# Kernel tuning notes

Hardware: AMD Instinct MI355X
Metric: run time of the kernel (lower is better)

The kernel has to match this reference:

```python
import jax, jax.numpy as jnp
import numpy as np

SPLIT = 8            # square window (split_size=[8,8], idx 0/1 identical)
DIM = 192
HEADS = 8
NH = HEADS // 2      # heads per branch
CH = DIM // 2        # channels per branch
HD = CH // NH        # head dim = 24
POS_DIM = (CH // 4) // 4  # DynamicPosBias hidden = 6
SCALE = HD ** -0.5
N = SPLIT * SPLIT    # window token count = 64


def _rel_index():
    c = np.arange(SPLIT)
    coords = np.stack(np.meshgrid(c, c, indexing='ij')).reshape(2, -1)
    rel = (coords[:, :, None] - coords[:, None, :]).transpose(1, 2, 0)
    rel[:, :, 0] += SPLIT - 1
    rel[:, :, 1] += SPLIT - 1
    rel[:, :, 0] *= 2 * SPLIT - 1
    return rel.sum(-1).reshape(-1)  # (N*N,) in [0, (2*SPLIT-1)^2)


def _rpe_biases():
    h = np.arange(1 - SPLIT, SPLIT)
    b = np.stack(np.meshgrid(h, h, indexing='ij')).reshape(2, -1).T
    return b.astype(np.float32)  # ((2*SPLIT-1)^2, 2) = (225, 2)


def _layernorm(x, g, b):
    mu = x.mean(-1, keepdims=True)
    var = ((x - mu) ** 2).mean(-1, keepdims=True)
    return (x - mu) / jnp.sqrt(var + 1e-5) * g + b


def setup_inputs() -> dict:
    key = jax.random.key(0)
    ks = jax.random.split(key, 12)
    s = 0.02
    inp = {
        'x': jax.random.normal(ks[0], (2, 65536, DIM), jnp.float32),
        'qkv_w': jax.random.normal(ks[1], (3 * DIM, DIM), jnp.float32) * s,
        'proj_w': jax.random.normal(ks[2], (DIM, DIM), jnp.float32) * s,
        'proj_b': jnp.zeros((DIM,), jnp.float32),
        # DynamicPosBias params, stacked over the 2 branches
        'pos_proj_w': jax.random.normal(ks[3], (2, POS_DIM, 2), jnp.float32) * s,
        'pos_proj_b': jnp.zeros((2, POS_DIM), jnp.float32),
        'ln1_g': jnp.ones((2, POS_DIM), jnp.float32),
        'ln1_b': jnp.zeros((2, POS_DIM), jnp.float32),
        'fc1_w': jax.random.normal(ks[4], (2, POS_DIM, POS_DIM), jnp.float32) * s,
        'fc1_b': jnp.zeros((2, POS_DIM), jnp.float32),
        'ln2_g': jnp.ones((2, POS_DIM), jnp.float32),
        'ln2_b': jnp.zeros((2, POS_DIM), jnp.float32),
        'fc2_w': jax.random.normal(ks[5], (2, POS_DIM, POS_DIM), jnp.float32) * s,
        'fc2_b': jnp.zeros((2, POS_DIM), jnp.float32),
        'ln3_g': jnp.ones((2, POS_DIM), jnp.float32),
        'ln3_b': jnp.zeros((2, POS_DIM), jnp.float32),
        'fc3_w': jax.random.normal(ks[6], (2, NH, POS_DIM), jnp.float32) * s,
        'fc3_b': jnp.zeros((2, NH), jnp.float32),
        'H': 256,
        'W': 256,
    }
    return inp


def reference(x, qkv_w, proj_w, proj_b, pos_proj_w, pos_proj_b,
              ln1_g, ln1_b, fc1_w, fc1_b, ln2_g, ln2_b, fc2_w, fc2_b,
              ln3_g, ln3_b, fc3_w, fc3_b, H, W):
    B, L, C = x.shape
    assert L == H * W and H % SPLIT == 0 and W % SPLIT == 0
    qkv = (x @ qkv_w.T).reshape(B, L, 3, C).transpose(2, 0, 1, 3)  # (3,B,L,C)
    rel_idx = jnp.asarray(_rel_index())
    rpe = jnp.asarray(_rpe_biases())
    outs = []
    for i in range(2):  # two channel-split branches
        qkv_i = qkv[..., i * CH:(i + 1) * CH]  # (3,B,L,CH)
        # window partition: (B,L,CH) -> (B*nW, NH, N, HD)
        def im2win(t):
            t = t.reshape(B, H // SPLIT, SPLIT, W // SPLIT, SPLIT, CH)
            t = t.transpose(0, 1, 3, 2, 4, 5).reshape(-1, N, NH, HD)
            return t.transpose(0, 2, 1, 3)
        q, k, v = im2win(qkv_i[0]), im2win(qkv_i[1]), im2win(qkv_i[2])
        attn = jnp.einsum('whnd,whmd->whnm', q * SCALE, k)  # (B*nW, NH, N, N)
        # dynamic relative position bias MLP (residual=False): pos3(pos2(pos1(proj(b))))
        pos = rpe @ pos_proj_w[i].T + pos_proj_b[i]
        pos = jax.nn.relu(_layernorm(pos, ln1_g[i], ln1_b[i])) @ fc1_w[i].T + fc1_b[i]
        pos = jax.nn.relu(_layernorm(pos, ln2_g[i], ln2_b[i])) @ fc2_w[i].T + fc2_b[i]
        pos = jax.nn.relu(_layernorm(pos, ln3_g[i], ln3_b[i])) @ fc3_w[i].T + fc3_b[i]  # (225, NH)
        bias = pos[rel_idx].reshape(N, N, NH).transpose(2, 0, 1)  # (NH, N, N)
        attn = jax.nn.softmax(attn + bias[None], axis=-1)
        o = jnp.einsum('whnm,whmd->whnd', attn, v)  # (B*nW, NH, N, HD)
        # windows2img back to (B, L, CH)
        o = o.transpose(0, 2, 1, 3).reshape(B, H // SPLIT, W // SPLIT, SPLIT, SPLIT, CH)
        o = o.transpose(0, 1, 3, 2, 4, 5).reshape(B, L, CH)
        outs.append(o)
    out = jnp.concatenate(outs, axis=-1)
    return out @ proj_w.T + proj_b
```

## Files before the change

### kernel.cpp

```cpp
#include <hip/hip_runtime.h>

typedef unsigned short u16;
typedef unsigned int u32;
typedef short short8v __attribute__((ext_vector_type(8)));
typedef float float4v __attribute__((ext_vector_type(4)));
typedef unsigned short ushort4v __attribute__((ext_vector_type(4)));

#define XLD   216
#define C1LD  392
#define VSLD  72
#define PLD   72
#define VS_OFF (64*C1LD)
#define LDS_U16 (VS_OFF + 8*24*VSLD)
#define LDS_BYTES (LDS_U16*2)

#define SC2 (0.20412414523193154f * 1.4426950408889634f)

__device__ __forceinline__ u16 f2bf(float f){
  unsigned u = __builtin_bit_cast(unsigned, f);
  return (u16)((u + 0x7FFFu + ((u >> 16) & 1u)) >> 16);
}
__device__ __forceinline__ void st4(u16* p, float4v v){
  ushort4v pk = { f2bf(v[0]), f2bf(v[1]), f2bf(v[2]), f2bf(v[3]) };
  *(ushort4v*)p = pk;
}

__global__ void prep_convert(const float* __restrict__ qkv_w, const float* __restrict__ proj_w,
                             u16* __restrict__ Wq, u16* __restrict__ Wp){
  int idx = blockIdx.x*blockDim.x + threadIdx.x;
  const int total = 110592 + 36864;
  for (; idx < total; idx += gridDim.x*blockDim.x){
    if (idx < 110592) Wq[idx] = f2bf(qkv_w[idx]);
    else              Wp[idx-110592] = f2bf(proj_w[idx-110592]);
  }
}

__device__ __forceinline__ void lnrelu6(float* v, const float* g, const float* b){
  float mu = (v[0]+v[1]+v[2]+v[3]+v[4]+v[5]) * (1.0f/6.0f);
  float var = 0.f;
  #pragma unroll
  for (int j=0;j<6;++j){ float d = v[j]-mu; var += d*d; }
  var *= (1.0f/6.0f);
  float inv = rsqrtf(var + 1e-5f);
  #pragma unroll
  for (int j=0;j<6;++j) v[j] = fmaxf((v[j]-mu)*inv*g[j] + b[j], 0.f);
}

__global__ void prep_bias(const float* __restrict__ ppw, const float* __restrict__ ppb,
                          const float* __restrict__ ln1g, const float* __restrict__ ln1b,
                          const float* __restrict__ fc1w, const float* __restrict__ fc1b,
                          const float* __restrict__ ln2g, const float* __restrict__ ln2b,
                          const float* __restrict__ fc2w, const float* __restrict__ fc2b,
                          const float* __restrict__ ln3g, const float* __restrict__ ln3b,
                          const float* __restrict__ fc3w, const float* __restrict__ fc3b,
                          float* __restrict__ biasT){
  __shared__ float pos3[2][225][4];
  const int t = threadIdx.x;
  if (t < 225){
    const float dy = (float)(t/15) - 7.0f;
    const float dx = (float)(t%15) - 7.0f;
    for (int i=0;i<2;++i){
      float v[6], y[6];
      #pragma unroll
      for (int j=0;j<6;++j)
        v[j] = dy*ppw[(i*6+j)*2+0] + dx*ppw[(i*6+j)*2+1] + ppb[i*6+j];
      lnrelu6(v, ln1g+i*6, ln1b+i*6);
      #pragma unroll
      for (int j=0;j<6;++j){
        float a = fc1b[i*6+j];
        #pragma unroll
        for (int k=0;k<6;++k) a += v[k]*fc1w[(i*6+j)*6+k];
        y[j] = a;
      }
      lnrelu6(y, ln2g+i*6, ln2b+i*6);
      #pragma unroll
      for (int j=0;j<6;++j){
        float a = fc2b[i*6+j];
        #pragma unroll
        for (int k=0;k<6;++k) a += y[k]*fc2w[(i*6+j)*6+k];
        v[j] = a;
      }
      lnrelu6(v, ln3g+i*6, ln3b+i*6);
      #pragma unroll
      for (int h=0;h<4;++h){
        float a = fc3b[i*4+h];
        #pragma unroll
        for (int k=0;k<6;++k) a += v[k]*fc3w[(i*4+h)*6+k];
        pos3[i][t][h] = a * 1.4426950408889634f;
      }
    }
  }
  __syncthreads();
  for (int idx = t; idx < 32768; idx += 256){
    int i  = idx >> 14;
    int hh = (idx >> 12) & 3;
    int n  = (idx >> 6) & 63;
    int m  = idx & 63;
    int tt = (((n>>3)-(m>>3)+7)*15) + ((n&7)-(m&7)+7);
    biasT[idx] = pos3[i][tt][hh];
  }
}

__device__ __forceinline__ void attn_head(u16* lds, u16* P,
                                          const short8v* qf, const short8v* kf,
                                          const float4v* bv, int hp, int q16, int g,
                                          float4v (&oo)[2][4]){
  const short8v z8 = {0,0,0,0,0,0,0,0};
  float4v s[4][4];
  #pragma unroll
  for (int kt=0;kt<4;++kt)
    #pragma unroll
    for (int mt=0;mt<4;++mt)
      s[kt][mt] = (float4v){0.f,0.f,0.f,0.f};
  __builtin_amdgcn_s_setprio(1);
  #pragma unroll
  for (int kt=0;kt<4;++kt)
    #pragma unroll
    for (int mt=0;mt<4;++mt)
      s[kt][mt] = __builtin_amdgcn_mfma_f32_16x16x32_bf16(kf[kt], qf[mt], s[kt][mt], 0,0,0);
  __builtin_amdgcn_s_setprio(0);
  #pragma unroll
  for (int kt=0;kt<4;++kt)
    #pragma unroll
    for (int mt=0;mt<4;++mt)
      s[kt][mt] = s[kt][mt]*SC2 + bv[kt*4+mt];
  float inv[4];
  #pragma unroll
  for (int mt=0;mt<4;++mt){
    float mx = s[0][mt][0];
    #pragma unroll
    for (int kt=0;kt<4;++kt)
      #pragma unroll
      for (int r=0;r<4;++r) mx = fmaxf(mx, s[kt][mt][r]);
    mx = fmaxf(mx, __shfl_xor(mx, 16));
    mx = fmaxf(mx, __shfl_xor(mx, 32));
    float sum = 0.f;
    #pragma unroll
    for (int kt=0;kt<4;++kt){
      float4v ev;
      #pragma unroll
      for (int r=0;r<4;++r){ float t2 = exp2f(s[kt][mt][r]-mx); ev[r] = t2; sum += t2; }
      st4(&P[(mt*16+q16)*PLD + kt*16 + g*4], ev);
    }
    sum += __shfl_xor(sum, 16);
    sum += __shfl_xor(sum, 32);
    inv[mt] = 1.0f / sum;
  }
  asm volatile("" ::: "memory");
  short8v vf[2][2];
  #pragma unroll
  for (int dt=0;dt<2;++dt){
    const int d  = dt*16 + q16;
    const int dc = (d < 24) ? d : 0;
    #pragma unroll
    for (int kc=0;kc<2;++kc){
      short8v vv = *(const short8v*)&lds[VS_OFF + (hp*24 + dc)*VSLD + kc*32 + g*8];
      vf[dt][kc] = (d < 24) ? vv : z8;
    }
  }
  #pragma unroll
  for (int dt=0;dt<2;++dt)
    #pragma unroll
    for (int mt=0;mt<4;++mt) oo[dt][mt] = (float4v){0.f,0.f,0.f,0.f};
  #pragma unroll
  for (int mt=0;mt<4;++mt){
    #pragma unroll
    for (int kc=0;kc<2;++kc){
      short8v pf = *(const short8v*)&P[(mt*16+q16)*PLD + kc*32 + g*8];
      __builtin_amdgcn_s_setprio(1);
      #pragma unroll
      for (int dt=0;dt<2;++dt)
        oo[dt][mt] = __builtin_amdgcn_mfma_f32_16x16x32_bf16(vf[dt][kc], pf, oo[dt][mt], 0,0,0);
      __builtin_amdgcn_s_setprio(0);
    }
  }
  #pragma unroll
  for (int dt=0;dt<2;++dt)
    #pragma unroll
    for (int mt=0;mt<4;++mt) oo[dt][mt] *= inv[mt];
}

__global__ __launch_bounds__(256, 2) void awa_main(
    const float* __restrict__ x, const u16* __restrict__ Wq,
    const u16* __restrict__ Wp, const float* __restrict__ proj_b,
    const float* __restrict__ biasT, float* __restrict__ out){
  extern __shared__ u16 lds[];
  const int tid  = threadIdx.x;
  const int wave = tid >> 6;
  const int lane = tid & 63;
  const int g    = lane >> 4;
  const int q16  = lane & 15;
  const int bid  = blockIdx.x;
  const int b    = bid >> 10;
  const int win  = bid & 1023;
  const int h1   = win >> 5, w1 = win & 31;
  const size_t xbase = ((size_t)b*65536u + (size_t)(h1*8)*256u + (size_t)(w1*8)) * 192u;
  const short8v z8 = {0,0,0,0,0,0,0,0};

  {
    float4v xr[12];
    #pragma unroll
    for (int it=0; it<12; ++it){
      int f = (tid + it*256) << 2;
      int rr = f/1536, rem = f - rr*1536, ss = rem/192, cc = rem - ss*192;
      xr[it] = *(const float4v*)(x + xbase + (size_t)((rr*256+ss)*192+cc));
    }
    #pragma unroll
    for (int it=0; it<12; ++it){
      int f = (tid + it*256) << 2;
      int rr = f/1536, rem = f - rr*1536, ss = rem/192, cc = rem - ss*192;
      st4(&lds[(rr*8+ss)*XLD + cc], xr[it]);
    }
  }
  __syncthreads();

  short8v xf[4][6];
  #pragma unroll
  for (int mt=0; mt<4; ++mt)
    #pragma unroll
    for (int kc=0; kc<6; ++kc)
      xf[mt][kc] = *(const short8v*)&lds[(mt*16+q16)*XLD + kc*32 + g*8];
  short8v wf[3][6];
  #pragma unroll
  for (int pb2=0; pb2<2; ++pb2){
    const u16* wb = Wq + (size_t)((wave + pb2*4)*16 + q16)*192 + g*8;
    #pragma unroll
    for (int kc=0;kc<6;++kc) wf[pb2][kc] = *(const short8v*)(wb + kc*32);
  }
  __syncthreads();

  #pragma unroll
  for (int t=0; t<9; ++t){
    const int nt = wave + t*4;
    if (t < 7){
      const u16* wb = Wq + (size_t)((nt+8)*16 + q16)*192 + g*8;
      #pragma unroll
      for (int kc=0;kc<6;++kc) wf[(t+2)%3][kc] = *(const short8v*)(wb + kc*32);
    }
    float4v acc[4];
    #pragma unroll
    for (int mt=0;mt<4;++mt) acc[mt] = (float4v){0.f,0.f,0.f,0.f};
    if (t < 6){
      #pragma unroll
      for (int kc=0; kc<6; ++kc)
        #pragma unroll
        for (int mt=0; mt<4; ++mt)
          acc[mt] = __builtin_amdgcn_mfma_f32_16x16x32_bf16(wf[t%3][kc], xf[mt][kc], acc[mt], 0,0,0);
      const int cb = nt*16 + g*4;
      #pragma unroll
      for (int mt=0; mt<4; ++mt)
        st4(&lds[(mt*16+q16)*C1LD + cb], acc[mt]);
    } else {
      #pragma unroll
      for (int kc=0; kc<6; ++kc)
        #pragma unroll
        for (int mt=0; mt<4; ++mt)
          acc[mt] = __builtin_amdgcn_mfma_f32_16x16x32_bf16(xf[mt][kc], wf[t%3][kc], acc[mt], 0,0,0);
      const int jj  = nt*16 + q16 - 384;
      const int ii2 = (jj >= 96) ? 1 : 0;
      const int c2  = jj - ii2*96;
      const int hh2 = c2 / 24;
      const int d   = c2 - hh2*24;
      const int vb  = VS_OFF + ((ii2*4 + hh2)*24 + d)*VSLD + g*4;
      #pragma unroll
      for (int mt=0; mt<4; ++mt)
        st4(&lds[vb + mt*16], acc[mt]);
    }
  }
  __syncthreads();

  short8v qf[2][4], kf[2][4];
  #pragma unroll
  for (int h=0; h<2; ++h){
    const int qb = h*96 + wave*24;
    #pragma unroll
    for (int mt=0; mt<4; ++mt){
      short8v a = *(const short8v*)&lds[(mt*16+q16)*C1LD + qb + g*8];
      short8v c = *(const short8v*)&lds[(mt*16+q16)*C1LD + 192 + qb + g*8];
      qf[h][mt] = (g==3) ? z8 : a;
      kf[h][mt] = (g==3) ? z8 : c;
    }
  }
  float4v bv0[16];
  {
    const float* bt = biasT + wave*4096;
    #pragma unroll
    for (int kt=0;kt<4;++kt)
      #pragma unroll
      for (int mt=0;mt<4;++mt)
        bv0[kt*4+mt] = *(const float4v*)&bt[(mt*16+q16)*64 + kt*16 + g*4];
  }
  __syncthreads();

  u16* P = &lds[wave*4608];
  float4v oo0[2][4], oo1[2][4];
  attn_head(lds, P, qf[0], kf[0], bv0, wave, q16, g, oo0);
  float4v bv1[16];
  {
    const float* bt = biasT + (4+wave)*4096;
    #pragma unroll
    for (int kt=0;kt<4;++kt)
      #pragma unroll
      for (int mt=0;mt<4;++mt)
        bv1[kt*4+mt] = *(const float4v*)&bt[(mt*16+q16)*64 + kt*16 + g*4];
  }
  attn_head(lds, P, qf[1], kf[1], bv1, 4+wave, q16, g, oo1);
  __syncthreads();

  #pragma unroll
  for (int h=0; h<2; ++h){
    const int cb = h*96 + wave*24;
    float4v (&oo)[2][4] = (h==0) ? oo0 : oo1;
    #pragma unroll
    for (int dt=0; dt<2; ++dt){
      if (dt==0 || g<2){
        #pragma unroll
        for (int mt=0; mt<4; ++mt)
          st4(&lds[(mt*16+q16)*XLD + cb + dt*16 + g*4], oo[dt][mt]);
      }
    }
  }
  short8v wp[3][6];
  #pragma unroll
  for (int pt=0; pt<3; ++pt){
    const u16* wb = Wp + (size_t)((wave + pt*4)*16 + q16)*192 + g*8;
    #pragma unroll
    for (int kc=0;kc<6;++kc) wp[pt][kc] = *(const short8v*)(wb + kc*32);
  }
  __syncthreads();

  short8v a2[4][6];
  #pragma unroll
  for (int mt=0; mt<4; ++mt)
    #pragma unroll
    for (int kc=0; kc<6; ++kc)
      a2[mt][kc] = *(const short8v*)&lds[(mt*16+q16)*XLD + kc*32 + g*8];
  #pragma unroll
  for (int t=0; t<3; ++t){
    const int nt = wave + t*4;
    float4v acc[4];
    #pragma unroll
    for (int mt=0;mt<4;++mt) acc[mt] = (float4v){0.f,0.f,0.f,0.f};
    #pragma unroll
    for (int kc=0; kc<6; ++kc)
      #pragma unroll
      for (int mt=0; mt<4; ++mt)
        acc[mt] = __builtin_amdgcn_mfma_f32_16x16x32_bf16(wp[t][kc], a2[mt][kc], acc[mt], 0,0,0);
    const int j0 = nt*16 + g*4;
    const float4v pb = *(const float4v*)(proj_b + j0);
    #pragma unroll
    for (int mt=0; mt<4; ++mt){
      const int tok = mt*16 + q16;
      const int l = ((h1*8 + (tok>>3)) << 8) + w1*8 + (tok & 7);
      float4v res = acc[mt] + pb;
      *(float4v*)(out + ((size_t)b*65536u + (size_t)l)*192u + j0) = res;
    }
  }
}

extern "C" void kernel_launch(void* const* d_in, const int* in_sizes, int n_in,
                              void* d_out, int out_size, void* d_ws, size_t ws_size,
                              hipStream_t stream){
  const float* x      = (const float*)d_in[0];
  const float* qkv_w  = (const float*)d_in[1];
  const float* proj_w = (const float*)d_in[2];
  const float* proj_b = (const float*)d_in[3];
  const float* ppw    = (const float*)d_in[4];
  const float* ppb    = (const float*)d_in[5];
  const float* ln1g   = (const float*)d_in[6];
  const float* ln1b   = (const float*)d_in[7];
  const float* fc1w   = (const float*)d_in[8];
  const float* fc1b   = (const float*)d_in[9];
  const float* ln2g   = (const float*)d_in[10];
  const float* ln2b   = (const float*)d_in[11];
  const float* fc2w   = (const float*)d_in[12];
  const float* fc2b   = (const float*)d_in[13];
  const float* ln3g   = (const float*)d_in[14];
  const float* ln3b   = (const float*)d_in[15];
  const float* fc3w   = (const float*)d_in[16];
  const float* fc3b   = (const float*)d_in[17];

  u16*   Wq    = (u16*)d_ws;
  u16*   Wp    = Wq + 110592;
  float* biasT = (float*)((char*)d_ws + 294912);

  prep_convert<<<144, 256, 0, stream>>>(qkv_w, proj_w, Wq, Wp);
  prep_bias<<<1, 256, 0, stream>>>(ppw, ppb, ln1g, ln1b, fc1w, fc1b,
                                   ln2g, ln2b, fc2w, fc2b, ln3g, ln3b,
                                   fc3w, fc3b, biasT);
  awa_main<<<2048, 256, LDS_BYTES, stream>>>(x, Wq, Wp, proj_b, biasT, (float*)d_out);
}
```

Baseline: 148.9 us.

## Restructure attention per head with padded QKV weights, bpermute P, smaller LDS

QKV weights are repacked into a per-head layout padded to 32 rows, so each wave computes its own head's Q, K and V right before attention and stages them in a small per-wave LDS arena instead of a full shared QKV buffer. The softmax probabilities are moved into MFMA operand layout with ds_bpermute instead of a round trip through LDS. Register arrays are cut by streaming weight and activation fragments per k-chunk. Together with the much smaller LDS footprint, this lets launch bounds rise to 3 blocks per CU. In exchange the padded weights add wasted MFMA work on the zero rows, and more weight loads come from global memory inside the loop.

```diff
diff --git a/kernel.cpp b/kernel.cpp
--- a/kernel.cpp
+++ b/kernel.cpp
@@ -5,13 +5,15 @@
 typedef short short8v __attribute__((ext_vector_type(8)));
 typedef float float4v __attribute__((ext_vector_type(4)));
 typedef unsigned short ushort4v __attribute__((ext_vector_type(4)));
-
-#define XLD   216
-#define C1LD  392
-#define VSLD  72
-#define PLD   72
-#define VS_OFF (64*C1LD)
-#define LDS_U16 (VS_OFF + 8*24*VSLD)
+typedef unsigned int uint2v __attribute__((ext_vector_type(2)));
+typedef unsigned int uint4v __attribute__((ext_vector_type(4)));
+
+#define XLD2  200
+#define QLD2  40
+#define VLD2  72
+#define ARENA_SZ 2560
+#define AR_OFF  12800
+#define LDS_U16 (AR_OFF + 4*ARENA_SZ)
 #define LDS_BYTES (LDS_U16*2)
 
 #define SC2 (0.20412414523193154f * 1.4426950408889634f)
@@ -24,14 +26,25 @@
   ushort4v pk = { f2bf(v[0]), f2bf(v[1]), f2bf(v[2]), f2bf(v[3]) };
   *(ushort4v*)p = pk;
 }
+__device__ __forceinline__ u32 pkbf(float a, float b){
+  return (u32)f2bf(a) | ((u32)f2bf(b) << 16);
+}
 
 __global__ void prep_convert(const float* __restrict__ qkv_w, const float* __restrict__ proj_w,
                              u16* __restrict__ Wq, u16* __restrict__ Wp){
   int idx = blockIdx.x*blockDim.x + threadIdx.x;
-  const int total = 110592 + 36864;
+  const int total = 147456 + 36864;
   for (; idx < total; idx += gridDim.x*blockDim.x){
-    if (idx < 110592) Wq[idx] = f2bf(qkv_w[idx]);
-    else              Wp[idx-110592] = f2bf(proj_w[idx-110592]);
+    if (idx < 147456){
+      int R = idx / 192, c = idx - R*192;
+      int part = R >> 8, hpd = R & 255, hp = hpd >> 5, d = hpd & 31;
+      float v = 0.f;
+      if (d < 24) v = qkv_w[(part*192 + (hp>>2)*96 + (hp&3)*24 + d)*192 + c];
+      Wq[idx] = f2bf(v);
+    } else {
+      int j = idx - 147456;
+      Wp[j] = f2bf(proj_w[j]);
+    }
   }
 }
 
@@ -101,86 +114,7 @@
   }
 }
 
-__device__ __forceinline__ void attn_head(u16* lds, u16* P,
-                                          const short8v* qf, const short8v* kf,
-                                          const float4v* bv, int hp, int q16, int g,
-                                          float4v (&oo)[2][4]){
-  const short8v z8 = {0,0,0,0,0,0,0,0};
-  float4v s[4][4];
-  #pragma unroll
-  for (int kt=0;kt<4;++kt)
-    #pragma unroll
-    for (int mt=0;mt<4;++mt)
-      s[kt][mt] = (float4v){0.f,0.f,0.f,0.f};
-  __builtin_amdgcn_s_setprio(1);
-  #pragma unroll
-  for (int kt=0;kt<4;++kt)
-    #pragma unroll
-    for (int mt=0;mt<4;++mt)
-      s[kt][mt] = __builtin_amdgcn_mfma_f32_16x16x32_bf16(kf[kt], qf[mt], s[kt][mt], 0,0,0);
-  __builtin_amdgcn_s_setprio(0);
-  #pragma unroll
-  for (int kt=0;kt<4;++kt)
-    #pragma unroll
-    for (int mt=0;mt<4;++mt)
-      s[kt][mt] = s[kt][mt]*SC2 + bv[kt*4+mt];
-  float inv[4];
-  #pragma unroll
-  for (int mt=0;mt<4;++mt){
-    float mx = s[0][mt][0];
-    #pragma unroll
-    for (int kt=0;kt<4;++kt)
-      #pragma unroll
-      for (int r=0;r<4;++r) mx = fmaxf(mx, s[kt][mt][r]);
-    mx = fmaxf(mx, __shfl_xor(mx, 16));
-    mx = fmaxf(mx, __shfl_xor(mx, 32));
-    float sum = 0.f;
-    #pragma unroll
-    for (int kt=0;kt<4;++kt){
-      float4v ev;
-      #pragma unroll
-      for (int r=0;r<4;++r){ float t2 = exp2f(s[kt][mt][r]-mx); ev[r] = t2; sum += t2; }
-      st4(&P[(mt*16+q16)*PLD + kt*16 + g*4], ev);
-    }
-    sum += __shfl_xor(sum, 16);
-    sum += __shfl_xor(sum, 32);
-    inv[mt] = 1.0f / sum;
-  }
-  asm volatile("" ::: "memory");
-  short8v vf[2][2];
-  #pragma unroll
-  for (int dt=0;dt<2;++dt){
-    const int d  = dt*16 + q16;
-    const int dc = (d < 24) ? d : 0;
-    #pragma unroll
-    for (int kc=0;kc<2;++kc){
-      short8v vv = *(const short8v*)&lds[VS_OFF + (hp*24 + dc)*VSLD + kc*32 + g*8];
-      vf[dt][kc] = (d < 24) ? vv : z8;
-    }
-  }
-  #pragma unroll
-  for (int dt=0;dt<2;++dt)
-    #pragma unroll
-    for (int mt=0;mt<4;++mt) oo[dt][mt] = (float4v){0.f,0.f,0.f,0.f};
-  #pragma unroll
-  for (int mt=0;mt<4;++mt){
-    #pragma unroll
-    for (int kc=0;kc<2;++kc){
-      short8v pf = *(const short8v*)&P[(mt*16+q16)*PLD + kc*32 + g*8];
-      __builtin_amdgcn_s_setprio(1);
-      #pragma unroll
-      for (int dt=0;dt<2;++dt)
-        oo[dt][mt] = __builtin_amdgcn_mfma_f32_16x16x32_bf16(vf[dt][kc], pf, oo[dt][mt], 0,0,0);
-      __builtin_amdgcn_s_setprio(0);
-    }
-  }
-  #pragma unroll
-  for (int dt=0;dt<2;++dt)
-    #pragma unroll
-    for (int mt=0;mt<4;++mt) oo[dt][mt] *= inv[mt];
-}
-
-__global__ __launch_bounds__(256, 2) void awa_main(
+__global__ __launch_bounds__(256, 3) void awa_main(
     const float* __restrict__ x, const u16* __restrict__ Wq,
     const u16* __restrict__ Wp, const float* __restrict__ proj_b,
     const float* __restrict__ biasT, float* __restrict__ out){
@@ -195,7 +129,7 @@
   const int win  = bid & 1023;
   const int h1   = win >> 5, w1 = win & 31;
   const size_t xbase = ((size_t)b*65536u + (size_t)(h1*8)*256u + (size_t)(w1*8)) * 192u;
-  const short8v z8 = {0,0,0,0,0,0,0,0};
+  u16* arena = &lds[AR_OFF + wave*ARENA_SZ];
 
   {
     float4v xr[12];
@@ -209,143 +143,195 @@
     for (int it=0; it<12; ++it){
       int f = (tid + it*256) << 2;
       int rr = f/1536, rem = f - rr*1536, ss = rem/192, cc = rem - ss*192;
-      st4(&lds[(rr*8+ss)*XLD + cc], xr[it]);
+      st4(&lds[(rr*8+ss)*XLD2 + cc], xr[it]);
     }
   }
   __syncthreads();
 
-  short8v xf[4][6];
-  #pragma unroll
-  for (int mt=0; mt<4; ++mt)
-    #pragma unroll
-    for (int kc=0; kc<6; ++kc)
-      xf[mt][kc] = *(const short8v*)&lds[(mt*16+q16)*XLD + kc*32 + g*8];
-  short8v wf[3][6];
-  #pragma unroll
-  for (int pb2=0; pb2<2; ++pb2){
-    const u16* wb = Wq + (size_t)((wave + pb2*4)*16 + q16)*192 + g*8;
-    #pragma unroll
-    for (int kc=0;kc<6;++kc) wf[pb2][kc] = *(const short8v*)(wb + kc*32);
-  }
-  __syncthreads();
-
-  #pragma unroll
-  for (int t=0; t<9; ++t){
-    const int nt = wave + t*4;
-    if (t < 7){
-      const u16* wb = Wq + (size_t)((nt+8)*16 + q16)*192 + g*8;
-      #pragma unroll
-      for (int kc=0;kc<6;++kc) wf[(t+2)%3][kc] = *(const short8v*)(wb + kc*32);
-    }
-    float4v acc[4];
-    #pragma unroll
-    for (int mt=0;mt<4;++mt) acc[mt] = (float4v){0.f,0.f,0.f,0.f};
-    if (t < 6){
-      #pragma unroll
-      for (int kc=0; kc<6; ++kc)
-        #pragma unroll
-        for (int mt=0; mt<4; ++mt)
-          acc[mt] = __builtin_amdgcn_mfma_f32_16x16x32_bf16(wf[t%3][kc], xf[mt][kc], acc[mt], 0,0,0);
-      const int cb = nt*16 + g*4;
-      #pragma unroll
-      for (int mt=0; mt<4; ++mt)
-        st4(&lds[(mt*16+q16)*C1LD + cb], acc[mt]);
-    } else {
-      #pragma unroll
-      for (int kc=0; kc<6; ++kc)
-        #pragma unroll
-        for (int mt=0; mt<4; ++mt)
-          acc[mt] = __builtin_amdgcn_mfma_f32_16x16x32_bf16(xf[mt][kc], wf[t%3][kc], acc[mt], 0,0,0);
-      const int jj  = nt*16 + q16 - 384;
-      const int ii2 = (jj >= 96) ? 1 : 0;
-      const int c2  = jj - ii2*96;
-      const int hh2 = c2 / 24;
-      const int d   = c2 - hh2*24;
-      const int vb  = VS_OFF + ((ii2*4 + hh2)*24 + d)*VSLD + g*4;
-      #pragma unroll
-      for (int mt=0; mt<4; ++mt)
-        st4(&lds[vb + mt*16], acc[mt]);
-    }
-  }
-  __syncthreads();
-
-  short8v qf[2][4], kf[2][4];
-  #pragma unroll
-  for (int h=0; h<2; ++h){
-    const int qb = h*96 + wave*24;
+  const int idxA = (((lane & 15) | ((lane & 16) << 1))) << 2;
+  const int idxB = idxA + 64;
+  const bool hi2 = (lane & 32) != 0;
+
+  uint2v po[2][2][4];
+
+  #pragma unroll
+  for (int h = 0; h < 2; ++h){
+    const int hp = h*4 + wave;
+    short8v qf[4], kf[4], vf[2][2];
+
+    #pragma unroll
+    for (int part = 0; part < 2; ++part){
+      float4v acc[2][4];
+      #pragma unroll
+      for (int tq=0;tq<2;++tq)
+        #pragma unroll
+        for (int mt=0;mt<4;++mt) acc[tq][mt] = (float4v){0.f,0.f,0.f,0.f};
+      const u16* w0 = Wq + (size_t)(part*256 + hp*32 + q16)*192 + g*8;
+      const u16* w1 = w0 + (size_t)16*192;
+      short8v wa0 = *(const short8v*)w0;
+      short8v wa1 = *(const short8v*)w1;
+      #pragma unroll
+      for (int kc = 0; kc < 6; ++kc){
+        short8v wb0, wb1;
+        if (kc < 5){ wb0 = *(const short8v*)(w0 + (kc+1)*32); wb1 = *(const short8v*)(w1 + (kc+1)*32); }
+        short8v xs[4];
+        #pragma unroll
+        for (int mt=0;mt<4;++mt)
+          xs[mt] = *(const short8v*)&lds[(mt*16+q16)*XLD2 + kc*32 + g*8];
+        #pragma unroll
+        for (int mt=0;mt<4;++mt){
+          acc[0][mt] = __builtin_amdgcn_mfma_f32_16x16x32_bf16(wa0, xs[mt], acc[0][mt], 0,0,0);
+          acc[1][mt] = __builtin_amdgcn_mfma_f32_16x16x32_bf16(wa1, xs[mt], acc[1][mt], 0,0,0);
+        }
+        wa0 = wb0; wa1 = wb1;
+      }
+      #pragma unroll
+      for (int tq=0;tq<2;++tq)
+        #pragma unroll
+        for (int mt=0;mt<4;++mt)
+          st4(&arena[(mt*16+q16)*QLD2 + tq*16 + g*4], acc[tq][mt]);
+      asm volatile("" ::: "memory");
+      #pragma unroll
+      for (int mt=0;mt<4;++mt){
+        short8v fr = *(const short8v*)&arena[(mt*16+q16)*QLD2 + g*8];
+        if (part == 0) qf[mt] = fr; else kf[mt] = fr;
+      }
+      asm volatile("" ::: "memory");
+    }
+
+    {
+      float4v acc[2][4];
+      #pragma unroll
+      for (int tv=0;tv<2;++tv)
+        #pragma unroll
+        for (int mt=0;mt<4;++mt) acc[tv][mt] = (float4v){0.f,0.f,0.f,0.f};
+      const u16* w0 = Wq + (size_t)(2*256 + hp*32 + q16)*192 + g*8;
+      const u16* w1 = w0 + (size_t)16*192;
+      short8v wa0 = *(const short8v*)w0;
+      short8v wa1 = *(const short8v*)w1;
+      #pragma unroll
+      for (int kc = 0; kc < 6; ++kc){
+        short8v wb0, wb1;
+        if (kc < 5){ wb0 = *(const short8v*)(w0 + (kc+1)*32); wb1 = *(const short8v*)(w1 + (kc+1)*32); }
+        short8v xs[4];
+        #pragma unroll
+        for (int mt=0;mt<4;++mt)
+          xs[mt] = *(const short8v*)&lds[(mt*16+q16)*XLD2 + kc*32 + g*8];
+        #pragma unroll
+        for (int mt=0;mt<4;++mt){
+          acc[0][mt] = __builtin_amdgcn_mfma_f32_16x16x32_bf16(xs[mt], wa0, acc[0][mt], 0,0,0);
+          acc[1][mt] = __builtin_amdgcn_mfma_f32_16x16x32_bf16(xs[mt], wa1, acc[1][mt], 0,0,0);
+        }
+        wa0 = wb0; wa1 = wb1;
+      }
+      #pragma unroll
+      for (int tv=0;tv<2;++tv)
+        #pragma unroll
+        for (int mt=0;mt<4;++mt)
+          st4(&arena[(tv*16+q16)*VLD2 + mt*16 + g*4], acc[tv][mt]);
+      asm volatile("" ::: "memory");
+      #pragma unroll
+      for (int dt=0;dt<2;++dt)
+        #pragma unroll
+        for (int kc=0;kc<2;++kc)
+          vf[dt][kc] = *(const short8v*)&arena[(dt*16+q16)*VLD2 + kc*32 + g*8];
+      asm volatile("" ::: "memory");
+    }
+
+    const float* bt = biasT + hp*4096;
     #pragma unroll
     for (int mt=0; mt<4; ++mt){
-      short8v a = *(const short8v*)&lds[(mt*16+q16)*C1LD + qb + g*8];
-      short8v c = *(const short8v*)&lds[(mt*16+q16)*C1LD + 192 + qb + g*8];
-      qf[h][mt] = (g==3) ? z8 : a;
-      kf[h][mt] = (g==3) ? z8 : c;
-    }
-  }
-  float4v bv0[16];
-  {
-    const float* bt = biasT + wave*4096;
-    #pragma unroll
-    for (int kt=0;kt<4;++kt)
-      #pragma unroll
-      for (int mt=0;mt<4;++mt)
-        bv0[kt*4+mt] = *(const float4v*)&bt[(mt*16+q16)*64 + kt*16 + g*4];
-  }
-  __syncthreads();
-
-  u16* P = &lds[wave*4608];
-  float4v oo0[2][4], oo1[2][4];
-  attn_head(lds, P, qf[0], kf[0], bv0, wave, q16, g, oo0);
-  float4v bv1[16];
-  {
-    const float* bt = biasT + (4+wave)*4096;
-    #pragma unroll
-    for (int kt=0;kt<4;++kt)
-      #pragma unroll
-      for (int mt=0;mt<4;++mt)
-        bv1[kt*4+mt] = *(const float4v*)&bt[(mt*16+q16)*64 + kt*16 + g*4];
-  }
-  attn_head(lds, P, qf[1], kf[1], bv1, 4+wave, q16, g, oo1);
+      float4v bv[4];
+      #pragma unroll
+      for (int kt=0;kt<4;++kt)
+        bv[kt] = *(const float4v*)&bt[(mt*16+q16)*64 + kt*16 + g*4];
+      float4v s[4];
+      #pragma unroll
+      for (int kt=0;kt<4;++kt) s[kt] = (float4v){0.f,0.f,0.f,0.f};
+      #pragma unroll
+      for (int kt=0;kt<4;++kt)
+        s[kt] = __builtin_amdgcn_mfma_f32_16x16x32_bf16(kf[kt], qf[mt], s[kt], 0,0,0);
+      #pragma unroll
+      for (int kt=0;kt<4;++kt) s[kt] = s[kt]*SC2 + bv[kt];
+      float mx = s[0][0];
+      #pragma unroll
+      for (int kt=0;kt<4;++kt)
+        #pragma unroll
+        for (int r=0;r<4;++r) mx = fmaxf(mx, s[kt][r]);
+      mx = fmaxf(mx, __shfl_xor(mx, 16));
+      mx = fmaxf(mx, __shfl_xor(mx, 32));
+      float sum = 0.f;
+      u32 pklo[4], pkhi[4];
+      #pragma unroll
+      for (int kt=0;kt<4;++kt){
+        float e0 = exp2f(s[kt][0]-mx), e1 = exp2f(s[kt][1]-mx);
+        float e2 = exp2f(s[kt][2]-mx), e3 = exp2f(s[kt][3]-mx);
+        sum += (e0+e1)+(e2+e3);
+        pklo[kt] = pkbf(e0, e1);
+        pkhi[kt] = pkbf(e2, e3);
+      }
+      sum += __shfl_xor(sum, 16);
+      sum += __shfl_xor(sum, 32);
+      const float inv = 1.0f / sum;
+      float4v o0 = (float4v){0.f,0.f,0.f,0.f};
+      float4v o1 = (float4v){0.f,0.f,0.f,0.f};
+      #pragma unroll
+      for (int kc=0;kc<2;++kc){
+        u32 a0 = (u32)__builtin_amdgcn_ds_bpermute(idxA, (int)pklo[2*kc]);
+        u32 a1 = (u32)__builtin_amdgcn_ds_bpermute(idxA, (int)pkhi[2*kc]);
+        u32 b0 = (u32)__builtin_amdgcn_ds_bpermute(idxB, (int)pklo[2*kc]);
+        u32 b1 = (u32)__builtin_amdgcn_ds_bpermute(idxB, (int)pkhi[2*kc]);
+        u32 c0 = (u32)__builtin_amdgcn_ds_bpermute(idxA, (int)pklo[2*kc+1]);
+        u32 c1 = (u32)__builtin_amdgcn_ds_bpermute(idxA, (int)pkhi[2*kc+1]);
+        u32 d0 = (u32)__builtin_amdgcn_ds_bpermute(idxB, (int)pklo[2*kc+1]);
+        u32 d1 = (u32)__builtin_amdgcn_ds_bpermute(idxB, (int)pkhi[2*kc+1]);
+        uint4v uv = { hi2 ? c0 : a0, hi2 ? c1 : a1, hi2 ? d0 : b0, hi2 ? d1 : b1 };
+        short8v pf = __builtin_bit_cast(short8v, uv);
+        o0 = __builtin_amdgcn_mfma_f32_16x16x32_bf16(vf[0][kc], pf, o0, 0,0,0);
+        o1 = __builtin_amdgcn_mfma_f32_16x16x32_bf16(vf[1][kc], pf, o1, 0,0,0);
+      }
+      o0 *= inv; o1 *= inv;
+      po[h][0][mt] = (uint2v){ pkbf(o0[0], o0[1]), pkbf(o0[2], o0[3]) };
+      po[h][1][mt] = (uint2v){ pkbf(o1[0], o1[1]), pkbf(o1[2], o1[3]) };
+    }
+  }
   __syncthreads();
 
   #pragma unroll
   for (int h=0; h<2; ++h){
     const int cb = h*96 + wave*24;
-    float4v (&oo)[2][4] = (h==0) ? oo0 : oo1;
     #pragma unroll
     for (int dt=0; dt<2; ++dt){
       if (dt==0 || g<2){
         #pragma unroll
         for (int mt=0; mt<4; ++mt)
-          st4(&lds[(mt*16+q16)*XLD + cb + dt*16 + g*4], oo[dt][mt]);
-      }
-    }
-  }
-  short8v wp[3][6];
-  #pragma unroll
-  for (int pt=0; pt<3; ++pt){
-    const u16* wb = Wp + (size_t)((wave + pt*4)*16 + q16)*192 + g*8;
-    #pragma unroll
-    for (int kc=0;kc<6;++kc) wp[pt][kc] = *(const short8v*)(wb + kc*32);
+          *(uint2v*)&lds[(mt*16+q16)*XLD2 + cb + dt*16 + g*4] = po[h][dt][mt];
+      }
+    }
   }
   __syncthreads();
 
-  short8v a2[4][6];
-  #pragma unroll
-  for (int mt=0; mt<4; ++mt)
-    #pragma unroll
-    for (int kc=0; kc<6; ++kc)
-      a2[mt][kc] = *(const short8v*)&lds[(mt*16+q16)*XLD + kc*32 + g*8];
   #pragma unroll
   for (int t=0; t<3; ++t){
     const int nt = wave + t*4;
+    const u16* wb = Wp + (size_t)(nt*16 + q16)*192 + g*8;
     float4v acc[4];
     #pragma unroll
     for (int mt=0;mt<4;++mt) acc[mt] = (float4v){0.f,0.f,0.f,0.f};
-    #pragma unroll
-    for (int kc=0; kc<6; ++kc)
+    short8v wa = *(const short8v*)wb;
+    #pragma unroll
+    for (int kc=0; kc<6; ++kc){
+      short8v wn;
+      if (kc < 5) wn = *(const short8v*)(wb + (kc+1)*32);
+      short8v a2[4];
+      #pragma unroll
+      for (int mt=0;mt<4;++mt)
+        a2[mt] = *(const short8v*)&lds[(mt*16+q16)*XLD2 + kc*32 + g*8];
       #pragma unroll
       for (int mt=0; mt<4; ++mt)
-        acc[mt] = __builtin_amdgcn_mfma_f32_16x16x32_bf16(wp[t][kc], a2[mt][kc], acc[mt], 0,0,0);
+        acc[mt] = __builtin_amdgcn_mfma_f32_16x16x32_bf16(wa, a2[mt], acc[mt], 0,0,0);
+      wa = wn;
+    }
     const int j0 = nt*16 + g*4;
     const float4v pb = *(const float4v*)(proj_b + j0);
     #pragma unroll
@@ -381,10 +367,10 @@
   const float* fc3b   = (const float*)d_in[17];
 
   u16*   Wq    = (u16*)d_ws;
-  u16*   Wp    = Wq + 110592;
-  float* biasT = (float*)((char*)d_ws + 294912);
-
-  prep_convert<<<144, 256, 0, stream>>>(qkv_w, proj_w, Wq, Wp);
+  u16*   Wp    = Wq + 147456;
+  float* biasT = (float*)((char*)d_ws + 368640);
+
+  prep_convert<<<180, 256, 0, stream>>>(qkv_w, proj_w, Wq, Wp);
   prep_bias<<<1, 256, 0, stream>>>(ppw, ppb, ln1g, ln1b, fc1w, fc1b,
                                    ln2g, ln2b, fc2w, fc2b, ln3g, ln3b,
                                    fc3w, fc3b, biasT);
```

After: 159.3 us. 7.0% more time.
